# Performance work log

Hardware: AMD Instinct MI355X
Metric: run time of the kernel (lower is better)

## Reference

```python
import jax, jax.numpy as jnp
import numpy as np

V = 257        # vocab size (prime -> multiplicative inverses exist mod V)
B = 64         # batch
L = 1024       # sequence length
TEMPERATURE = 1.0


def one_hot_argmax(logits, temperature):
    # hard one-hot forward, softmax-temperature backward (straight-through)
    hard = jax.nn.one_hot(jnp.argmax(logits, axis=-1), logits.shape[-1], dtype=logits.dtype)
    soft = jax.nn.softmax(logits / temperature, axis=-1)
    return soft + jax.lax.stop_gradient(hard - soft)


def setup_inputs() -> dict:
    key = jax.random.key(0)
    k1, k2, k3 = jax.random.split(key, 3)
    idx = jax.random.randint(k1, (B, L), 0, V)
    x = jax.nn.one_hot(idx, V, dtype=jnp.float32)          # [B, L, V] hard one-hot
    W = jax.random.normal(k2, (V, 2 * V), jnp.float32) * 0.05
    b = jax.random.normal(k3, (2 * V,), jnp.float32) * 0.05
    # extended-Euclid inverse table (V prime -> Fermat: a^(V-2) mod V); inv(0):=0
    inv = np.array([0] + [pow(a, V - 2, V) for a in range(1, V)], dtype=np.int32)
    return {"x": x, "W": W, "b": b, "inv_table": jnp.asarray(inv)}


def reference(x, W, b, inv_table):
    dtype = x.dtype
    u = jnp.arange(V)
    # one_hot_minus: shift_matrix[u, v] = shift[(v - u) % V]
    minus_idx = (u[None, :] - u[:, None]) % V              # [V, V]
    # one_hot_multiply: for a != 0, scaled[a, u] = inputs[(u * inv(a)) % V]
    vidx = (u[None, :] * inv_table[:, None]) % V           # [V, V]
    notzero = (u != 0).astype(dtype)[None, :, None]        # zero out scale-by-0 row

    @jax.checkpoint
    def step(prev, x_t):
        # prev: [B, V] previous output one-hot; x_t: [B, V] current input one-hot
        net = prev @ W + b                                  # [B, 2V] causal masked layer
        loc_logits, scale_logits = jnp.split(net, 2, axis=-1)
        loc = one_hot_argmax(loc_logits, TEMPERATURE)       # [B, V]
        scale = one_hot_argmax(scale_logits, TEMPERATURE)   # [B, V]
        # multiplicative inverse of scale in one-hot space (non-differentiable, as in py_func)
        inv_scale = jax.nn.one_hot(inv_table[jnp.argmax(scale, axis=-1)], V, dtype=dtype)
        # (x_t - loc) % V in one-hot space: einsum('...v,...uv->...u') with rolled loc
        shifted = jnp.einsum('bv,buv->bu', x_t, loc[:, minus_idx])
        # (shifted * inv_scale) % V in one-hot space
        scaled = shifted[:, vidx] * notzero                 # [B, V, V]
        out = jnp.einsum('ba,bau->bu', inv_scale, scaled)   # [B, V]
        return out, out

    init = jnp.zeros((x.shape[0], V), dtype)
    _, ys = jax.lax.scan(step, init, jnp.swapaxes(x, 0, 1))  # scan over L
    return jnp.swapaxes(ys, 0, 1)                            # [B, L, V]
```

## Files before the change

### kernel.cpp

```cpp
#include <hip/hip_runtime.h>
#include <stdint.h>

#define V 257
#define NB 64
#define L 1024
#define ZERO_STATE 257
#define NSTATE 258
#define CHUNKS 32
#define CLEN 32

__device__ __forceinline__ int gstep(const uint32_t* __restrict__ tbl, int p, int x) {
    uint32_t e = tbl[p];
    int ia  = (int)(e >> 16);
    int loc = (int)(e & 0xffff);
    int s = x - loc;
    s += (s >> 31) & V;
    int n = s * ia;
    int m = (n & 255) - (n >> 8);
    m += (m >> 31) & V;
    return (ia == 0) ? ZERO_STATE : m;
}

__global__ void build_table(const float* __restrict__ W, const float* __restrict__ bias,
                            const int* __restrict__ inv_table, uint32_t* __restrict__ gtable) {
    int p = blockIdx.x;
    int lane = threadIdx.x;
    const float* wrow = (p < V) ? (W + (size_t)p * (2 * V)) : nullptr;
    float bestL = -INFINITY; int idxL = 0;
    float bestS = -INFINITY; int idxS = 0;
    for (int j = lane; j < V; j += 64) {
        float vl = wrow ? (wrow[j] + bias[j]) : bias[j];
        float vs = wrow ? (wrow[V + j] + bias[V + j]) : bias[V + j];
        if (vl > bestL) { bestL = vl; idxL = j; }
        if (vs > bestS) { bestS = vs; idxS = j; }
    }
    for (int off = 32; off >= 1; off >>= 1) {
        float oL = __shfl_down(bestL, off); int oiL = __shfl_down(idxL, off);
        float oS = __shfl_down(bestS, off); int oiS = __shfl_down(idxS, off);
        if (oL > bestL || (oL == bestL && oiL < idxL)) { bestL = oL; idxL = oiL; }
        if (oS > bestS || (oS == bestS && oiS < idxS)) { bestS = oS; idxS = oiS; }
    }
    if (lane == 0) {
        int ia = inv_table[idxS];
        gtable[p] = (uint32_t)idxL | ((uint32_t)ia << 16);
    }
}

__global__ void extract_idx(const float4* __restrict__ x4, uint16_t* __restrict__ xidx, int n4) {
    int stride = gridDim.x * blockDim.x;
    for (int i = blockIdx.x * blockDim.x + threadIdx.x; i < n4; i += stride) {
        float4 v = x4[i];
        int j = i * 4;
        if (v.x == 1.0f) { int r = j / V;       xidx[r] = (uint16_t)(j     - r * V); }
        if (v.y == 1.0f) { int r = (j + 1) / V; xidx[r] = (uint16_t)(j + 1 - r * V); }
        if (v.z == 1.0f) { int r = (j + 2) / V; xidx[r] = (uint16_t)(j + 2 - r * V); }
        if (v.w == 1.0f) { int r = (j + 3) / V; xidx[r] = (uint16_t)(j + 3 - r * V); }
    }
}

__global__ void phase1(const uint32_t* __restrict__ gtable, const uint16_t* __restrict__ xidx,
                       uint16_t* __restrict__ f) {
    __shared__ uint32_t tbl[NSTATE];
    __shared__ uint16_t xs[CLEN];
    int bc = blockIdx.x;
    int b = bc / CHUNKS, c = bc % CHUNKS;
    int tid = threadIdx.x;
    for (int j = tid; j < NSTATE; j += 128) tbl[j] = gtable[j];
    if (tid < CLEN) xs[tid] = xidx[b * L + c * CLEN + tid];
    __syncthreads();
    int p0 = tid;
    int p1 = tid + 128;
    int p2 = (tid + 256 < NSTATE) ? tid + 256 : 0;
    #pragma unroll 4
    for (int k = 0; k < CLEN; ++k) {
        int x = xs[k];
        p0 = gstep(tbl, p0, x);
        p1 = gstep(tbl, p1, x);
        p2 = gstep(tbl, p2, x);
    }
    uint16_t* frow = f + (size_t)bc * NSTATE;
    frow[tid] = (uint16_t)p0;
    frow[tid + 128] = (uint16_t)p1;
    if (tid < 2) frow[tid + 256] = (uint16_t)p2;
}

__global__ void phase23(const uint32_t* __restrict__ gtable, const uint16_t* __restrict__ xidx,
                        const uint16_t* __restrict__ f, uint16_t* __restrict__ oidx) {
    __shared__ uint32_t tbl[NSTATE];
    __shared__ uint16_t fl[CHUNKS * NSTATE];
    __shared__ uint16_t xs[L];
    __shared__ uint16_t os[L];
    __shared__ uint16_t entry[CHUNKS];
    int b = blockIdx.x, tid = threadIdx.x;
    for (int j = tid; j < NSTATE; j += 256) tbl[j] = gtable[j];
    for (int j = tid; j < CHUNKS * NSTATE; j += 256) fl[j] = f[(size_t)b * CHUNKS * NSTATE + j];
    for (int j = tid; j < L; j += 256) xs[j] = xidx[b * L + j];
    __syncthreads();
    if (tid == 0) {
        int st = ZERO_STATE;
        for (int c = 0; c < CHUNKS; ++c) { entry[c] = (uint16_t)st; st = fl[c * NSTATE + st]; }
    }
    __syncthreads();
    if (tid < CHUNKS) {
        int p = entry[tid];
        int base = tid * CLEN;
        for (int k = 0; k < CLEN; ++k) {
            int x = xs[base + k];
            uint32_t e = tbl[p];
            int ia  = (int)(e >> 16);
            int loc = (int)(e & 0xffff);
            if (ia == 0) {
                os[base + k] = 0xFFFF;
                p = ZERO_STATE;
            } else {
                int s = x - loc;
                s += (s >> 31) & V;
                int n = s * ia;
                int m = (n & 255) - (n >> 8);
                m += (m >> 31) & V;
                os[base + k] = (uint16_t)m;
                p = m;
            }
        }
    }
    __syncthreads();
    for (int j = tid; j < L; j += 256) oidx[b * L + j] = os[j];
}

__global__ void write_out(const uint16_t* __restrict__ oidx, float4* __restrict__ out, int n4) {
    int stride = gridDim.x * blockDim.x;
    for (int i = blockIdx.x * blockDim.x + threadIdx.x; i < n4; i += stride) {
        int j = i * 4;
        float4 v;
        { int r = j / V;            int c = j - r * V;      v.x = (c == (int)oidx[r]) ? 1.0f : 0.0f; }
        { int jj = j + 1; int r = jj / V; int c = jj - r * V; v.y = (c == (int)oidx[r]) ? 1.0f : 0.0f; }
        { int jj = j + 2; int r = jj / V; int c = jj - r * V; v.z = (c == (int)oidx[r]) ? 1.0f : 0.0f; }
        { int jj = j + 3; int r = jj / V; int c = jj - r * V; v.w = (c == (int)oidx[r]) ? 1.0f : 0.0f; }
        out[i] = v;
    }
}

extern "C" void kernel_launch(void* const* d_in, const int* in_sizes, int n_in,
                              void* d_out, int out_size, void* d_ws, size_t ws_size,
                              hipStream_t stream) {
    const float* x    = (const float*)d_in[0];
    const float* W    = (const float*)d_in[1];
    const float* bias = (const float*)d_in[2];
    const int*   inv  = (const int*)d_in[3];
    float* out = (float*)d_out;

    uint8_t* ws = (uint8_t*)d_ws;
    uint32_t* gtable = (uint32_t*)ws;
    uint16_t* xidx   = (uint16_t*)(ws + 4096);
    uint16_t* oidx   = (uint16_t*)(ws + 4096 + NB * L * 2);
    uint16_t* f      = (uint16_t*)(ws + 4096 + 2 * NB * L * 2);

    int n4 = NB * L * V / 4;

    build_table<<<NSTATE, 64, 0, stream>>>(W, bias, inv, gtable);
    extract_idx<<<2048, 256, 0, stream>>>((const float4*)x, xidx, n4);
    phase1<<<NB * CHUNKS, 128, 0, stream>>>(gtable, xidx, f);
    phase23<<<NB, 256, 0, stream>>>(gtable, xidx, f, oidx);
    write_out<<<2048, 256, 0, stream>>>(oidx, (float4*)out, n4);
}
```

Measured before the change: 141.3 us.

## Fuse table build with index extraction; memset output and scatter ones

Merges build_table and extract_idx into one launch, using separate block ranges, to save a kernel launch. Replaces the write_out kernel with a hipMemsetAsync of the output followed by a scatter of 1.0 values from the solve kernel, dropping the oidx workspace round trip. The memset still writes the full dense output. The scattered writes are uncoalesced but few, and the table-building blocks now launch 256 threads with 192 of them idle.

```diff
diff --git a/kernel.cpp b/kernel.cpp
--- a/kernel.cpp
+++ b/kernel.cpp
@@ -8,6 +8,7 @@
 #define NSTATE 258
 #define CHUNKS 32
 #define CLEN 32
+#define EXTRACT_BLOCKS 2048
 
 __device__ __forceinline__ int gstep(const uint32_t* __restrict__ tbl, int p, int x) {
     uint32_t e = tbl[p];
@@ -21,34 +22,36 @@
     return (ia == 0) ? ZERO_STATE : m;
 }
 
-__global__ void build_table(const float* __restrict__ W, const float* __restrict__ bias,
-                            const int* __restrict__ inv_table, uint32_t* __restrict__ gtable) {
-    int p = blockIdx.x;
-    int lane = threadIdx.x;
-    const float* wrow = (p < V) ? (W + (size_t)p * (2 * V)) : nullptr;
-    float bestL = -INFINITY; int idxL = 0;
-    float bestS = -INFINITY; int idxS = 0;
-    for (int j = lane; j < V; j += 64) {
-        float vl = wrow ? (wrow[j] + bias[j]) : bias[j];
-        float vs = wrow ? (wrow[V + j] + bias[V + j]) : bias[V + j];
-        if (vl > bestL) { bestL = vl; idxL = j; }
-        if (vs > bestS) { bestS = vs; idxS = j; }
+__global__ void prep(const float* __restrict__ W, const float* __restrict__ bias,
+                     const int* __restrict__ inv_table, const float4* __restrict__ x4,
+                     uint32_t* __restrict__ gtable, uint16_t* __restrict__ xidx, int n4) {
+    if (blockIdx.x < NSTATE) {
+        int lane = threadIdx.x;
+        if (lane >= 64) return;
+        int p = blockIdx.x;
+        const float* wrow = (p < V) ? (W + (size_t)p * (2 * V)) : nullptr;
+        float bestL = -INFINITY; int idxL = 0;
+        float bestS = -INFINITY; int idxS = 0;
+        for (int j = lane; j < V; j += 64) {
+            float vl = wrow ? (wrow[j] + bias[j]) : bias[j];
+            float vs = wrow ? (wrow[V + j] + bias[V + j]) : bias[V + j];
+            if (vl > bestL) { bestL = vl; idxL = j; }
+            if (vs > bestS) { bestS = vs; idxS = j; }
+        }
+        for (int off = 32; off >= 1; off >>= 1) {
+            float oL = __shfl_down(bestL, off); int oiL = __shfl_down(idxL, off);
+            float oS = __shfl_down(bestS, off); int oiS = __shfl_down(idxS, off);
+            if (oL > bestL || (oL == bestL && oiL < idxL)) { bestL = oL; idxL = oiL; }
+            if (oS > bestS || (oS == bestS && oiS < idxS)) { bestS = oS; idxS = oiS; }
+        }
+        if (lane == 0) {
+            int ia = inv_table[idxS];
+            gtable[p] = (uint32_t)idxL | ((uint32_t)ia << 16);
+        }
+        return;
     }
-    for (int off = 32; off >= 1; off >>= 1) {
-        float oL = __shfl_down(bestL, off); int oiL = __shfl_down(idxL, off);
-        float oS = __shfl_down(bestS, off); int oiS = __shfl_down(idxS, off);
-        if (oL > bestL || (oL == bestL && oiL < idxL)) { bestL = oL; idxL = oiL; }
-        if (oS > bestS || (oS == bestS && oiS < idxS)) { bestS = oS; idxS = oiS; }
-    }
-    if (lane == 0) {
-        int ia = inv_table[idxS];
-        gtable[p] = (uint32_t)idxL | ((uint32_t)ia << 16);
-    }
-}
-
-__global__ void extract_idx(const float4* __restrict__ x4, uint16_t* __restrict__ xidx, int n4) {
-    int stride = gridDim.x * blockDim.x;
-    for (int i = blockIdx.x * blockDim.x + threadIdx.x; i < n4; i += stride) {
+    int stride = EXTRACT_BLOCKS * blockDim.x;
+    for (int i = (blockIdx.x - NSTATE) * blockDim.x + threadIdx.x; i < n4; i += stride) {
         float4 v = x4[i];
         int j = i * 4;
         if (v.x == 1.0f) { int r = j / V;       xidx[r] = (uint16_t)(j     - r * V); }
@@ -84,8 +87,8 @@
     if (tid < 2) frow[tid + 256] = (uint16_t)p2;
 }
 
-__global__ void phase23(const uint32_t* __restrict__ gtable, const uint16_t* __restrict__ xidx,
-                        const uint16_t* __restrict__ f, uint16_t* __restrict__ oidx) {
+__global__ void solve(const uint32_t* __restrict__ gtable, const uint16_t* __restrict__ xidx,
+                      const uint16_t* __restrict__ f, float* __restrict__ out) {
     __shared__ uint32_t tbl[NSTATE];
     __shared__ uint16_t fl[CHUNKS * NSTATE];
     __shared__ uint16_t xs[L];
@@ -124,19 +127,9 @@
         }
     }
     __syncthreads();
-    for (int j = tid; j < L; j += 256) oidx[b * L + j] = os[j];
-}
-
-__global__ void write_out(const uint16_t* __restrict__ oidx, float4* __restrict__ out, int n4) {
-    int stride = gridDim.x * blockDim.x;
-    for (int i = blockIdx.x * blockDim.x + threadIdx.x; i < n4; i += stride) {
-        int j = i * 4;
-        float4 v;
-        { int r = j / V;            int c = j - r * V;      v.x = (c == (int)oidx[r]) ? 1.0f : 0.0f; }
-        { int jj = j + 1; int r = jj / V; int c = jj - r * V; v.y = (c == (int)oidx[r]) ? 1.0f : 0.0f; }
-        { int jj = j + 2; int r = jj / V; int c = jj - r * V; v.z = (c == (int)oidx[r]) ? 1.0f : 0.0f; }
-        { int jj = j + 3; int r = jj / V; int c = jj - r * V; v.w = (c == (int)oidx[r]) ? 1.0f : 0.0f; }
-        out[i] = v;
+    for (int t = tid; t < L; t += 256) {
+        int v = os[t];
+        if (v != 0xFFFF) out[((size_t)b * L + t) * V + v] = 1.0f;
     }
 }
 
@@ -152,14 +145,13 @@
     uint8_t* ws = (uint8_t*)d_ws;
     uint32_t* gtable = (uint32_t*)ws;
     uint16_t* xidx   = (uint16_t*)(ws + 4096);
-    uint16_t* oidx   = (uint16_t*)(ws + 4096 + NB * L * 2);
-    uint16_t* f      = (uint16_t*)(ws + 4096 + 2 * NB * L * 2);
+    uint16_t* f      = (uint16_t*)(ws + 4096 + NB * L * 2);
 
     int n4 = NB * L * V / 4;
 
-    build_table<<<NSTATE, 64, 0, stream>>>(W, bias, inv, gtable);
-    extract_idx<<<2048, 256, 0, stream>>>((const float4*)x, xidx, n4);
+    hipMemsetAsync(d_out, 0, (size_t)out_size * sizeof(float), stream);
+    prep<<<NSTATE + EXTRACT_BLOCKS, 256, 0, stream>>>(W, bias, inv, (const float4*)x,
+                                                      gtable, xidx, n4);
     phase1<<<NB * CHUNKS, 128, 0, stream>>>(gtable, xidx, f);
-    phase23<<<NB, 256, 0, stream>>>(gtable, xidx, f, oidx);
-    write_out<<<2048, 256, 0, stream>>>(oidx, (float4*)out, n4);
+    solve<<<NB, 256, 0, stream>>>(gtable, xidx, f, out);
 }
```

Measured after the change: 148.7 us. 5.2% more time.

## Fuse all five kernels into one cooperative persistent kernel with grid syncs

Applied to the files above, without the earlier changes.

Replaces the five separate launches (table build, index extraction, chunk transition maps, chunk stitching, one-hot write) with a single cooperative kernel of 1024 blocks. Phases are separated by grid-wide barriers, and each block handles two chunk units in the transition phase. The aim is to cut per-launch overhead and inter-kernel gaps. The trade-offs are grid.sync cost, a fixed grid size for the memory-bound phases, and a large shared-memory footprint that may limit occupancy.

```diff
diff --git a/kernel.cpp b/kernel.cpp
--- a/kernel.cpp
+++ b/kernel.cpp
@@ -1,5 +1,8 @@
 #include <hip/hip_runtime.h>
+#include <hip/hip_cooperative_groups.h>
 #include <stdint.h>
+
+namespace cg = cooperative_groups;
 
 #define V 257
 #define NB 64
@@ -8,6 +11,8 @@
 #define NSTATE 258
 #define CHUNKS 32
 #define CLEN 32
+#define GRID_BLOCKS 1024
+#define BLOCK_THREADS 256
 
 __device__ __forceinline__ int gstep(const uint32_t* __restrict__ tbl, int p, int x) {
     uint32_t e = tbl[p];
@@ -21,34 +26,46 @@
     return (ia == 0) ? ZERO_STATE : m;
 }
 
-__global__ void build_table(const float* __restrict__ W, const float* __restrict__ bias,
-                            const int* __restrict__ inv_table, uint32_t* __restrict__ gtable) {
-    int p = blockIdx.x;
-    int lane = threadIdx.x;
-    const float* wrow = (p < V) ? (W + (size_t)p * (2 * V)) : nullptr;
-    float bestL = -INFINITY; int idxL = 0;
-    float bestS = -INFINITY; int idxS = 0;
-    for (int j = lane; j < V; j += 64) {
-        float vl = wrow ? (wrow[j] + bias[j]) : bias[j];
-        float vs = wrow ? (wrow[V + j] + bias[V + j]) : bias[V + j];
-        if (vl > bestL) { bestL = vl; idxL = j; }
-        if (vs > bestS) { bestS = vs; idxS = j; }
+__global__ void __launch_bounds__(BLOCK_THREADS, 4)
+mega(const float* __restrict__ W, const float* __restrict__ bias,
+     const int* __restrict__ inv_table, const float4* __restrict__ x4,
+     float* __restrict__ out, uint32_t* __restrict__ gtable,
+     uint16_t* __restrict__ xidx, uint16_t* __restrict__ f,
+     uint16_t* __restrict__ oidx, int n4) {
+    cg::grid_group grid = cg::this_grid();
+    __shared__ uint32_t s_tbl[NSTATE];
+    __shared__ uint16_t s_fl[CHUNKS * NSTATE];
+    __shared__ uint16_t s_xs[L];
+    __shared__ uint16_t s_os[L];
+    __shared__ uint16_t s_entry[CHUNKS];
+
+    const int tid = threadIdx.x, bk = blockIdx.x;
+    const int gtid = bk * BLOCK_THREADS + tid;
+    const int gstride = GRID_BLOCKS * BLOCK_THREADS;
+
+    if (bk < NSTATE && tid < 64) {
+        int p = bk;
+        const float* wrow = (p < V) ? (W + (size_t)p * (2 * V)) : nullptr;
+        float bestL = -INFINITY; int idxL = 0;
+        float bestS = -INFINITY; int idxS = 0;
+        for (int j = tid; j < V; j += 64) {
+            float vl = wrow ? (wrow[j] + bias[j]) : bias[j];
+            float vs = wrow ? (wrow[V + j] + bias[V + j]) : bias[V + j];
+            if (vl > bestL) { bestL = vl; idxL = j; }
+            if (vs > bestS) { bestS = vs; idxS = j; }
+        }
+        for (int off = 32; off >= 1; off >>= 1) {
+            float oL = __shfl_down(bestL, off); int oiL = __shfl_down(idxL, off);
+            float oS = __shfl_down(bestS, off); int oiS = __shfl_down(idxS, off);
+            if (oL > bestL || (oL == bestL && oiL < idxL)) { bestL = oL; idxL = oiL; }
+            if (oS > bestS || (oS == bestS && oiS < idxS)) { bestS = oS; idxS = oiS; }
+        }
+        if (tid == 0) {
+            int ia = inv_table[idxS];
+            gtable[p] = (uint32_t)idxL | ((uint32_t)ia << 16);
+        }
     }
-    for (int off = 32; off >= 1; off >>= 1) {
-        float oL = __shfl_down(bestL, off); int oiL = __shfl_down(idxL, off);
-        float oS = __shfl_down(bestS, off); int oiS = __shfl_down(idxS, off);
-        if (oL > bestL || (oL == bestL && oiL < idxL)) { bestL = oL; idxL = oiL; }
-        if (oS > bestS || (oS == bestS && oiS < idxS)) { bestS = oS; idxS = oiS; }
-    }
-    if (lane == 0) {
-        int ia = inv_table[idxS];
-        gtable[p] = (uint32_t)idxL | ((uint32_t)ia << 16);
-    }
-}
-
-__global__ void extract_idx(const float4* __restrict__ x4, uint16_t* __restrict__ xidx, int n4) {
-    int stride = gridDim.x * blockDim.x;
-    for (int i = blockIdx.x * blockDim.x + threadIdx.x; i < n4; i += stride) {
+    for (int i = gtid; i < n4; i += gstride) {
         float4 v = x4[i];
         int j = i * 4;
         if (v.x == 1.0f) { int r = j / V;       xidx[r] = (uint16_t)(j     - r * V); }
@@ -56,87 +73,77 @@
         if (v.z == 1.0f) { int r = (j + 2) / V; xidx[r] = (uint16_t)(j + 2 - r * V); }
         if (v.w == 1.0f) { int r = (j + 3) / V; xidx[r] = (uint16_t)(j + 3 - r * V); }
     }
-}
+    grid.sync();
 
-__global__ void phase1(const uint32_t* __restrict__ gtable, const uint16_t* __restrict__ xidx,
-                       uint16_t* __restrict__ f) {
-    __shared__ uint32_t tbl[NSTATE];
-    __shared__ uint16_t xs[CLEN];
-    int bc = blockIdx.x;
-    int b = bc / CHUNKS, c = bc % CHUNKS;
-    int tid = threadIdx.x;
-    for (int j = tid; j < NSTATE; j += 128) tbl[j] = gtable[j];
-    if (tid < CLEN) xs[tid] = xidx[b * L + c * CLEN + tid];
-    __syncthreads();
-    int p0 = tid;
-    int p1 = tid + 128;
-    int p2 = (tid + 256 < NSTATE) ? tid + 256 : 0;
-    #pragma unroll 4
-    for (int k = 0; k < CLEN; ++k) {
-        int x = xs[k];
-        p0 = gstep(tbl, p0, x);
-        p1 = gstep(tbl, p1, x);
-        p2 = gstep(tbl, p2, x);
+    {
+        int h = tid >> 7, t = tid & 127;
+        int unit = bk * 2 + h;
+        int b = unit >> 5, c = unit & 31;
+        for (int j = tid; j < NSTATE; j += BLOCK_THREADS) s_tbl[j] = gtable[j];
+        if (t < CLEN) s_xs[h * CLEN + t] = xidx[b * L + c * CLEN + t];
+        __syncthreads();
+        int p0 = t;
+        int p1 = t + 128;
+        int p2 = (t < 2) ? t + 256 : 0;
+        #pragma unroll 4
+        for (int k = 0; k < CLEN; ++k) {
+            int x = s_xs[h * CLEN + k];
+            p0 = gstep(s_tbl, p0, x);
+            p1 = gstep(s_tbl, p1, x);
+            p2 = gstep(s_tbl, p2, x);
+        }
+        uint16_t* frow = f + (size_t)unit * NSTATE;
+        frow[t] = (uint16_t)p0;
+        frow[t + 128] = (uint16_t)p1;
+        if (t < 2) frow[t + 256] = (uint16_t)p2;
     }
-    uint16_t* frow = f + (size_t)bc * NSTATE;
-    frow[tid] = (uint16_t)p0;
-    frow[tid + 128] = (uint16_t)p1;
-    if (tid < 2) frow[tid + 256] = (uint16_t)p2;
-}
+    grid.sync();
 
-__global__ void phase23(const uint32_t* __restrict__ gtable, const uint16_t* __restrict__ xidx,
-                        const uint16_t* __restrict__ f, uint16_t* __restrict__ oidx) {
-    __shared__ uint32_t tbl[NSTATE];
-    __shared__ uint16_t fl[CHUNKS * NSTATE];
-    __shared__ uint16_t xs[L];
-    __shared__ uint16_t os[L];
-    __shared__ uint16_t entry[CHUNKS];
-    int b = blockIdx.x, tid = threadIdx.x;
-    for (int j = tid; j < NSTATE; j += 256) tbl[j] = gtable[j];
-    for (int j = tid; j < CHUNKS * NSTATE; j += 256) fl[j] = f[(size_t)b * CHUNKS * NSTATE + j];
-    for (int j = tid; j < L; j += 256) xs[j] = xidx[b * L + j];
-    __syncthreads();
-    if (tid == 0) {
-        int st = ZERO_STATE;
-        for (int c = 0; c < CHUNKS; ++c) { entry[c] = (uint16_t)st; st = fl[c * NSTATE + st]; }
-    }
-    __syncthreads();
-    if (tid < CHUNKS) {
-        int p = entry[tid];
-        int base = tid * CLEN;
-        for (int k = 0; k < CLEN; ++k) {
-            int x = xs[base + k];
-            uint32_t e = tbl[p];
-            int ia  = (int)(e >> 16);
-            int loc = (int)(e & 0xffff);
-            if (ia == 0) {
-                os[base + k] = 0xFFFF;
-                p = ZERO_STATE;
-            } else {
-                int s = x - loc;
-                s += (s >> 31) & V;
-                int n = s * ia;
-                int m = (n & 255) - (n >> 8);
-                m += (m >> 31) & V;
-                os[base + k] = (uint16_t)m;
-                p = m;
+    if (bk < NB) {
+        for (int j = tid; j < CHUNKS * NSTATE; j += BLOCK_THREADS)
+            s_fl[j] = f[(size_t)bk * CHUNKS * NSTATE + j];
+        for (int j = tid; j < L; j += BLOCK_THREADS) s_xs[j] = xidx[bk * L + j];
+        __syncthreads();
+        if (tid == 0) {
+            int st = ZERO_STATE;
+            for (int c = 0; c < CHUNKS; ++c) { s_entry[c] = (uint16_t)st; st = s_fl[c * NSTATE + st]; }
+        }
+        __syncthreads();
+        if (tid < CHUNKS) {
+            int p = s_entry[tid];
+            int base = tid * CLEN;
+            for (int k = 0; k < CLEN; ++k) {
+                int x = s_xs[base + k];
+                uint32_t e = s_tbl[p];
+                int ia  = (int)(e >> 16);
+                int loc = (int)(e & 0xffff);
+                if (ia == 0) {
+                    s_os[base + k] = 0xFFFF;
+                    p = ZERO_STATE;
+                } else {
+                    int s = x - loc;
+                    s += (s >> 31) & V;
+                    int n = s * ia;
+                    int m = (n & 255) - (n >> 8);
+                    m += (m >> 31) & V;
+                    s_os[base + k] = (uint16_t)m;
+                    p = m;
+                }
             }
         }
+        __syncthreads();
+        for (int j = tid; j < L; j += BLOCK_THREADS) oidx[bk * L + j] = s_os[j];
     }
-    __syncthreads();
-    for (int j = tid; j < L; j += 256) oidx[b * L + j] = os[j];
-}
+    grid.sync();
 
-__global__ void write_out(const uint16_t* __restrict__ oidx, float4* __restrict__ out, int n4) {
-    int stride = gridDim.x * blockDim.x;
-    for (int i = blockIdx.x * blockDim.x + threadIdx.x; i < n4; i += stride) {
+    for (int i = gtid; i < n4; i += gstride) {
         int j = i * 4;
         float4 v;
-        { int r = j / V;            int c = j - r * V;      v.x = (c == (int)oidx[r]) ? 1.0f : 0.0f; }
+        { int r = j / V;            int c = j - r * V;        v.x = (c == (int)oidx[r]) ? 1.0f : 0.0f; }
         { int jj = j + 1; int r = jj / V; int c = jj - r * V; v.y = (c == (int)oidx[r]) ? 1.0f : 0.0f; }
         { int jj = j + 2; int r = jj / V; int c = jj - r * V; v.z = (c == (int)oidx[r]) ? 1.0f : 0.0f; }
         { int jj = j + 3; int r = jj / V; int c = jj - r * V; v.w = (c == (int)oidx[r]) ? 1.0f : 0.0f; }
-        out[i] = v;
+        ((float4*)out)[i] = v;
     }
 }
 
@@ -156,10 +163,10 @@
     uint16_t* f      = (uint16_t*)(ws + 4096 + 2 * NB * L * 2);
 
     int n4 = NB * L * V / 4;
+    const float4* x4 = (const float4*)x;
 
-    build_table<<<NSTATE, 64, 0, stream>>>(W, bias, inv, gtable);
-    extract_idx<<<2048, 256, 0, stream>>>((const float4*)x, xidx, n4);
-    phase1<<<NB * CHUNKS, 128, 0, stream>>>(gtable, xidx, f);
-    phase23<<<NB, 256, 0, stream>>>(gtable, xidx, f, oidx);
-    write_out<<<2048, 256, 0, stream>>>(oidx, (float4*)out, n4);
+    void* args[] = { (void*)&W, (void*)&bias, (void*)&inv, (void*)&x4, (void*)&out,
+                     (void*)&gtable, (void*)&xidx, (void*)&f, (void*)&oidx, (void*)&n4 };
+    hipLaunchCooperativeKernel((const void*)mega, dim3(GRID_BLOCKS), dim3(BLOCK_THREADS),
+                               args, 0, stream);
 }
```

Result: slower. 456.1 us (+222.7%).
